# Performance work log

Hardware: AMD Instinct MI355X
Metric: run time of the kernel (lower is better)

The kernel has to match this reference:

```python
import jax, jax.numpy as jnp
import numpy as np

B, S, D = 4, 2048, 2048  # batch, seq, input_dim == state_dim
N = D

def setup_inputs() -> dict:
    key = jax.random.key(0)
    ks = jax.random.split(key, 6)
    x = jax.random.normal(ks[0], (B, S, D), dtype=jnp.float32)
    W_dt = jax.random.normal(ks[1], (N, D), dtype=jnp.float32) / np.sqrt(D)
    b_dt = jnp.ones((N,), dtype=jnp.float32)  # dt_proj.bias.fill_(1.0)
    W_B = jax.random.normal(ks[2], (N, D), dtype=jnp.float32) / np.sqrt(D)
    W_C = jax.random.normal(ks[3], (D, N), dtype=jnp.float32) / np.sqrt(N)
    A_log = jax.random.normal(ks[4], (N,), dtype=jnp.float32) * 0.5 - 1.0
    D_skip = jnp.zeros((D,), dtype=jnp.float32)
    return {"x": x, "W_dt": W_dt, "b_dt": b_dt, "W_B": W_B, "W_C": W_C,
            "A_log": A_log, "D_skip": D_skip}

def reference(x, W_dt, b_dt, W_B, W_C, A_log, D_skip):
    # dt = softplus(x @ W_dt^T + b_dt) -> [B,S,N]
    dt = jax.nn.softplus(jnp.einsum('bsd,nd->bsn', x, W_dt) + b_dt)
    Bp = jnp.einsum('bsd,nd->bsn', x, W_B)          # [B,S,N]
    A = -jnp.exp(A_log)                              # [N]
    A_bar = jnp.exp(dt * A)                          # [B,S,N]
    inputs = (dt * Bp) * x                           # B_bar * x (N == D)
    # selective scan: h_t = A_bar_t * h_{t-1} + inputs_t
    h0 = jnp.zeros((x.shape[0], A_log.shape[0]), dtype=x.dtype)
    def step(h, ab_u):
        ab, u = ab_u
        h = ab * h + u
        return h, h
    # scan over time axis: move S to leading axis
    _, h_all = jax.lax.scan(step, h0,
                            (jnp.swapaxes(A_bar, 0, 1), jnp.swapaxes(inputs, 0, 1)))
    h_all = jnp.swapaxes(h_all, 0, 1)                # [B,S,N]
    out = jnp.einsum('bsn,dn->bsd', h_all, W_C) + D_skip * x
    return out
```

## Files before the change

### kernel.cpp

```cpp
#include <hip/hip_runtime.h>

#define SEQ    2048
#define DIM    2048
#define NBATCH 4
#define MTOT   (NBATCH * SEQ)
#define CHUNKS 32
#define CLEN   (SEQ / CHUNKS)
#define NBM    (MTOT / 128)
#define TILE_E (128 * 32)

typedef __bf16 bf16_t;
typedef __bf16 bf16x8 __attribute__((ext_vector_type(8)));
typedef float  f32x4  __attribute__((ext_vector_type(4)));
typedef unsigned short u16x4 __attribute__((ext_vector_type(4)));
typedef unsigned short u16x2 __attribute__((ext_vector_type(2)));

__device__ __forceinline__ unsigned short f2bf_rne(float f) {
    unsigned int u = __float_as_uint(f);
    u += 0x7fffu + ((u >> 16) & 1u);
    return (unsigned short)(u >> 16);
}
__device__ __forceinline__ float bf2f(unsigned short v) {
    return __uint_as_float((unsigned int)v << 16);
}

__global__ void k_convert(const float* __restrict__ src,
                          unsigned short* __restrict__ dst, int n4) {
    int i = blockIdx.x * blockDim.x + threadIdx.x;
    if (i >= n4) return;
    f32x4 v = ((const f32x4*)src)[i];
    u16x4 o;
    o[0] = f2bf_rne(v[0]); o[1] = f2bf_rne(v[1]);
    o[2] = f2bf_rne(v[2]); o[3] = f2bf_rne(v[3]);
    ((u16x4*)dst)[i] = o;
}

__global__ void k_convert_ilv(const float* __restrict__ src,
                              unsigned short* __restrict__ dst, int n4, int phase) {
    int i = blockIdx.x * blockDim.x + threadIdx.x;
    if (i >= n4) return;
    const int R4 = DIM / 4;
    int nrow = i / R4;
    int dcol = i - nrow * R4;
    f32x4 v = ((const f32x4*)src)[i];
    u16x4 o;
    o[0] = f2bf_rne(v[0]); o[1] = f2bf_rne(v[1]);
    o[2] = f2bf_rne(v[2]); o[3] = f2bf_rne(v[3]);
    ((u16x4*)dst)[(2 * nrow + phase) * R4 + dcol] = o;
}

__global__ void k_prep_a(const float* __restrict__ A_log, float* __restrict__ negA, int n) {
    int i = blockIdx.x * blockDim.x + threadIdx.x;
    if (i < n) negA[i] = -__expf(A_log[i]);
}

__device__ __forceinline__ void stage_tile(const bf16_t* __restrict__ g, long rowbase,
                                           int K, int k0, bf16_t* lds,
                                           int wave, int lane) {
    const int rl     = lane >> 2;
    const int gchunk = (lane & 3) ^ ((lane >> 3) & 3);
#pragma unroll
    for (int q = 0; q < 2; q++) {
        const bf16_t* ga = g + (rowbase + wave * 32 + q * 16 + rl) * (long)K
                             + k0 + gchunk * 8;
        __builtin_amdgcn_global_load_lds(
            (const __attribute__((address_space(1))) void*)ga,
            (__attribute__((address_space(3))) void*)((char*)lds + (wave * 32 + q * 16) * 64),
            16, 0, 0);
    }
}

template <int KITERS>
__device__ __forceinline__ void gemm_main(const bf16_t* __restrict__ A,
                                          const bf16_t* __restrict__ Bm,
                                          int K, long arow0, long brow0,
                                          bf16_t* As, bf16_t* Bs,
                                          f32x4 acc[4][4],
                                          int wave, int lane, int wm, int wn) {
    const int l15  = lane & 15;
    const int quad = lane >> 4;
    const int swz  = (quad ^ ((l15 >> 1) & 3)) * 8;

    stage_tile(A,  arow0, K, 0, As, wave, lane);
    stage_tile(Bm, brow0, K, 0, Bs, wave, lane);

    for (int i = 0; i < KITERS; ++i) {
        asm volatile("s_waitcnt vmcnt(0)\n\ts_barrier" ::: "memory");
        const bf16_t* ap = As + (i & 1) * TILE_E;
        const bf16_t* bp = Bs + (i & 1) * TILE_E;
        bf16x8 af[4], bfr[4];
#pragma unroll
        for (int t = 0; t < 4; t++) {
            af[t]  = *(const bf16x8*)(ap + (wm * 64 + t * 16 + l15) * 32 + swz);
            bfr[t] = *(const bf16x8*)(bp + (wn * 64 + t * 16 + l15) * 32 + swz);
        }
        if (i + 1 < KITERS) {
            stage_tile(A,  arow0, K, (i + 1) * 32, As + ((i + 1) & 1) * TILE_E, wave, lane);
            stage_tile(Bm, brow0, K, (i + 1) * 32, Bs + ((i + 1) & 1) * TILE_E, wave, lane);
        }
#pragma unroll
        for (int t = 0; t < 4; t++)
#pragma unroll
            for (int j = 0; j < 4; j++)
                acc[t][j] = __builtin_amdgcn_mfma_f32_16x16x32_bf16(
                    af[t], bfr[j], acc[t][j], 0, 0, 0);
    }
}

__global__ __launch_bounds__(256)
void k_gemm_fused(const bf16_t* __restrict__ A, const bf16_t* __restrict__ Wcat,
                  const float* __restrict__ x, const float* __restrict__ b_dt,
                  const float* __restrict__ negA,
                  unsigned short* __restrict__ abuf, unsigned short* __restrict__ ubuf) {
    __shared__ __align__(16) bf16_t As[2 * TILE_E];
    __shared__ __align__(16) bf16_t Bs[2 * TILE_E];

    const int tid  = threadIdx.x;
    const int lane = tid & 63;
    const int wave = tid >> 6;
    const int wm   = wave >> 1;
    const int wn   = wave & 1;
    int flat = blockIdx.y * gridDim.x + blockIdx.x;
    int bm = flat % NBM;
    int bn = flat / NBM;

    f32x4 acc[4][4];
#pragma unroll
    for (int i = 0; i < 4; i++)
#pragma unroll
        for (int j = 0; j < 4; j++) acc[i][j] = (f32x4){0.f, 0.f, 0.f, 0.f};

    gemm_main<DIM / 32>(A, Wcat, DIM, (long)bm * 128, (long)bn * 128,
                        As, Bs, acc, wave, lane, wm, wn);

    const int l15  = lane & 15;
    const int quad = lane >> 4;
    const int odd  = l15 & 1;
#pragma unroll
    for (int i = 0; i < 4; i++) {
#pragma unroll
        for (int j = 0; j < 4; j++) {
#pragma unroll
            for (int r = 0; r < 4; r++) {
                float v = acc[i][j][r];
                float w = __shfl_xor(v, 1);
                float dtpre = odd ? w : v;
                float bpv   = odd ? v : w;
                long row = (long)bm * 128 + wm * 64 + i * 16 + quad * 4 + r;
                int  col = bn * 128 + wn * 64 + j * 16 + l15;
                int  n   = col >> 1;
                float z  = dtpre + b_dt[n];
                float dt = (z > 15.f) ? z : __logf(1.f + __expf(z));
                float a  = __expf(negA[n] * dt);
                float u  = dt * bpv * x[row * DIM + n];
                long idx = row * DIM + n;
                if (odd) ubuf[idx] = f2bf_rne(u); else abuf[idx] = f2bf_rne(a);
            }
        }
    }
}

__global__ __launch_bounds__(256)
void k_gemm_bt(const bf16_t* __restrict__ A, const bf16_t* __restrict__ Bm,
               float* __restrict__ C, int N, int K,
               const float* __restrict__ skip, const float* __restrict__ xres) {
    __shared__ __align__(16) bf16_t As[2 * TILE_E];
    __shared__ __align__(16) bf16_t Bs[2 * TILE_E];

    const int tid  = threadIdx.x;
    const int lane = tid & 63;
    const int wave = tid >> 6;
    const int wm   = wave >> 1;
    const int wn   = wave & 1;
    int flat = blockIdx.y * gridDim.x + blockIdx.x;
    int bm = flat % NBM;
    int bn = flat / NBM;

    f32x4 acc[4][4];
#pragma unroll
    for (int i = 0; i < 4; i++)
#pragma unroll
        for (int j = 0; j < 4; j++) acc[i][j] = (f32x4){0.f, 0.f, 0.f, 0.f};

    gemm_main<DIM / 32>(A, Bm, K, (long)bm * 128, (long)bn * 128,
                        As, Bs, acc, wave, lane, wm, wn);

    const int l15  = lane & 15;
    const int quad = lane >> 4;
#pragma unroll
    for (int i = 0; i < 4; i++) {
#pragma unroll
        for (int j = 0; j < 4; j++) {
#pragma unroll
            for (int r = 0; r < 4; r++) {
                long row = (long)bm * 128 + wm * 64 + i * 16 + quad * 4 + r;
                long col = (long)bn * 128 + wn * 64 + j * 16 + l15;
                long idx = row * (long)N + col;
                float v = acc[i][j][r];
                if (skip) v += skip[col] * xres[idx];
                C[idx] = v;
            }
        }
    }
}

__global__ void k_scan1(const unsigned short* __restrict__ a,
                        const unsigned short* __restrict__ u,
                        float* __restrict__ P, float* __restrict__ V) {
    int t  = blockIdx.x * blockDim.x + threadIdx.x;
    int n2 = t & (DIM / 2 - 1);
    int c  = (t >> 10) & (CHUNKS - 1);
    int b  = t >> 15;
    long base = ((long)b * SEQ + (long)c * CLEN) * DIM + n2 * 2;
    float p0 = 1.f, v0 = 0.f, p1 = 1.f, v1 = 0.f;
    for (int s = 0; s < CLEN; s++) {
        u16x2 av = *(const u16x2*)(a + base + (long)s * DIM);
        u16x2 uv = *(const u16x2*)(u + base + (long)s * DIM);
        float a0 = bf2f(av[0]), a1 = bf2f(av[1]);
        v0 = a0 * v0 + bf2f(uv[0]);  p0 *= a0;
        v1 = a1 * v1 + bf2f(uv[1]);  p1 *= a1;
    }
    long pidx = ((long)b * CHUNKS + c) * DIM + n2 * 2;
    *(float2*)(P + pidx) = make_float2(p0, p1);
    *(float2*)(V + pidx) = make_float2(v0, v1);
}

__global__ void k_scan2(const float* __restrict__ P, const float* __restrict__ V,
                        float* __restrict__ carry) {
    int t = blockIdx.x * blockDim.x + threadIdx.x;
    int n = t & (DIM - 1);
    int b = t >> 11;
    float H = 0.f;
    for (int c = 0; c < CHUNKS; c++) {
        long idx = ((long)b * CHUNKS + c) * DIM + n;
        carry[idx] = H;
        H = P[idx] * H + V[idx];
    }
}

__global__ void k_scan3(const unsigned short* __restrict__ a,
                        const unsigned short* __restrict__ u,
                        const float* __restrict__ carry,
                        unsigned short* __restrict__ h) {
    int t  = blockIdx.x * blockDim.x + threadIdx.x;
    int n2 = t & (DIM / 2 - 1);
    int c  = (t >> 10) & (CHUNKS - 1);
    int b  = t >> 15;
    long base = ((long)b * SEQ + (long)c * CLEN) * DIM + n2 * 2;
    long cidx = ((long)b * CHUNKS + c) * DIM + n2 * 2;
    float2 Hc = *(const float2*)(carry + cidx);
    float H0 = Hc.x, H1 = Hc.y;
    for (int s = 0; s < CLEN; s++) {
        u16x2 av = *(const u16x2*)(a + base + (long)s * DIM);
        u16x2 uv = *(const u16x2*)(u + base + (long)s * DIM);
        H0 = bf2f(av[0]) * H0 + bf2f(uv[0]);
        H1 = bf2f(av[1]) * H1 + bf2f(uv[1]);
        u16x2 o; o[0] = f2bf_rne(H0); o[1] = f2bf_rne(H1);
        *(u16x2*)(h + base + (long)s * DIM) = o;
    }
}

extern "C" void kernel_launch(void* const* d_in, const int* in_sizes, int n_in,
                              void* d_out, int out_size, void* d_ws, size_t ws_size,
                              hipStream_t stream) {
    const float* x      = (const float*)d_in[0];
    const float* W_dt   = (const float*)d_in[1];
    const float* b_dt   = (const float*)d_in[2];
    const float* W_B    = (const float*)d_in[3];
    const float* W_C    = (const float*)d_in[4];
    const float* A_log  = (const float*)d_in[5];
    const float* D_skip = (const float*)d_in[6];
    float* out = (float*)d_out;

    char* ws = (char*)d_ws;
    size_t off = 0;
    auto alloc = [&](size_t bytes) -> char* {
        char* p = ws + off;
        off += (bytes + 255) & ~(size_t)255;
        return p;
    };
    unsigned short* xb   = (unsigned short*)alloc((size_t)MTOT * DIM * 2);
    unsigned short* wcat = (unsigned short*)alloc((size_t)2 * DIM * DIM * 2);
    unsigned short* wcb  = (unsigned short*)alloc((size_t)DIM * DIM * 2);
    unsigned short* abuf = (unsigned short*)alloc((size_t)MTOT * DIM * 2);
    unsigned short* ubuf = (unsigned short*)alloc((size_t)MTOT * DIM * 2);
    float* P     = (float*)alloc((size_t)NBATCH * CHUNKS * DIM * 4);
    float* V     = (float*)alloc((size_t)NBATCH * CHUNKS * DIM * 4);
    float* carry = (float*)alloc((size_t)NBATCH * CHUNKS * DIM * 4);
    float* negA  = (float*)alloc((size_t)DIM * 4);

    const int n4x = MTOT * DIM / 4;
    const int n4w = DIM * DIM / 4;
    k_convert<<<n4x / 256, 256, 0, stream>>>(x, xb, n4x);
    k_convert_ilv<<<n4w / 256, 256, 0, stream>>>(W_dt, wcat, n4w, 0);
    k_convert_ilv<<<n4w / 256, 256, 0, stream>>>(W_B,  wcat, n4w, 1);
    k_convert<<<n4w / 256, 256, 0, stream>>>(W_C, wcb, n4w);
    k_prep_a<<<DIM / 256, 256, 0, stream>>>(A_log, negA, DIM);

    dim3 fgrid(2 * DIM / 128, MTOT / 128);
    k_gemm_fused<<<fgrid, 256, 0, stream>>>((const bf16_t*)xb, (const bf16_t*)wcat,
                                            x, b_dt, negA, abuf, ubuf);

    const int scan2_threads = NBATCH * CHUNKS * DIM / 2;
    k_scan1<<<scan2_threads / 256, 256, 0, stream>>>(abuf, ubuf, P, V);
    k_scan2<<<(NBATCH * DIM) / 256, 256, 0, stream>>>(P, V, carry);
    k_scan3<<<scan2_threads / 256, 256, 0, stream>>>(abuf, ubuf, carry, xb );

    dim3 ggrid(DIM / 128, MTOT / 128);
    k_gemm_bt<<<ggrid, 256, 0, stream>>>((const bf16_t*)xb, (const bf16_t*)wcb,
                                         out, DIM, DIM, D_skip, x);
}
```

Baseline: 558.1 us.

## Switch GEMMs to 256x256 tiles with 8-wave ping-pong pipeline and block swizzle

Both bf16 GEMMs move from 128x128 tiles with 4 waves to 256x256 tiles with 8 waves and 64-wide K steps. Global-to-LDS staging is interleaved between MFMA groups across four half-buffers with explicit vmcnt waits, barriers and setprio. Block indices are remapped so neighbouring blocks share rows of A and B for better L2 reuse. The aim is higher arithmetic intensity and overlap of loads with MFMA, at the cost of more registers and LDS per block, fewer blocks in the grid, and more intricate synchronisation.

After: 498.4 us. 1.12x faster.

```diff
diff --git a/kernel.cpp b/kernel.cpp
--- a/kernel.cpp
+++ b/kernel.cpp
@@ -6,8 +6,7 @@
 #define MTOT   (NBATCH * SEQ)
 #define CHUNKS 32
 #define CLEN   (SEQ / CHUNKS)
-#define NBM    (MTOT / 128)
-#define TILE_E (128 * 32)
+#define HT_ELEMS (256 * 32)
 
 typedef __bf16 bf16_t;
 typedef __bf16 bf16x8 __attribute__((ext_vector_type(8)));
@@ -54,7 +53,7 @@
     if (i < n) negA[i] = -__expf(A_log[i]);
 }
 
-__device__ __forceinline__ void stage_tile(const bf16_t* __restrict__ g, long rowbase,
+__device__ __forceinline__ void stage_half(const bf16_t* __restrict__ g, long rowbase,
                                            int K, int k0, bf16_t* lds,
                                            int wave, int lane) {
     const int rl     = lane >> 2;
@@ -70,74 +69,138 @@
     }
 }
 
-template <int KITERS>
-__device__ __forceinline__ void gemm_main(const bf16_t* __restrict__ A,
-                                          const bf16_t* __restrict__ Bm,
-                                          int K, long arow0, long brow0,
-                                          bf16_t* As, bf16_t* Bs,
-                                          f32x4 acc[4][4],
-                                          int wave, int lane, int wm, int wn) {
+#define MFMA_B16(a, b, c) __builtin_amdgcn_mfma_f32_16x16x32_bf16(a, b, c, 0, 0, 0)
+#define BAR_MEM asm volatile("s_barrier" ::: "memory")
+
+template <int KTILES>
+__device__ __forceinline__ void gemm256_main(const bf16_t* __restrict__ A,
+                                             const bf16_t* __restrict__ Bm,
+                                             int K, long arow0, long brow0,
+                                             bf16_t* As, bf16_t* Bs,
+                                             f32x4 acc[8][4],
+                                             int wave, int lane, int wm, int wn) {
     const int l15  = lane & 15;
     const int quad = lane >> 4;
     const int swz  = (quad ^ ((l15 >> 1) & 3)) * 8;
-
-    stage_tile(A,  arow0, K, 0, As, wave, lane);
-    stage_tile(Bm, brow0, K, 0, Bs, wave, lane);
-
-    for (int i = 0; i < KITERS; ++i) {
-        asm volatile("s_waitcnt vmcnt(0)\n\ts_barrier" ::: "memory");
-        const bf16_t* ap = As + (i & 1) * TILE_E;
-        const bf16_t* bp = Bs + (i & 1) * TILE_E;
-        bf16x8 af[4], bfr[4];
-#pragma unroll
-        for (int t = 0; t < 4; t++) {
-            af[t]  = *(const bf16x8*)(ap + (wm * 64 + t * 16 + l15) * 32 + swz);
-            bfr[t] = *(const bf16x8*)(bp + (wn * 64 + t * 16 + l15) * 32 + swz);
-        }
-        if (i + 1 < KITERS) {
-            stage_tile(A,  arow0, K, (i + 1) * 32, As + ((i + 1) & 1) * TILE_E, wave, lane);
-            stage_tile(Bm, brow0, K, (i + 1) * 32, Bs + ((i + 1) & 1) * TILE_E, wave, lane);
-        }
-#pragma unroll
-        for (int t = 0; t < 4; t++)
-#pragma unroll
-            for (int j = 0; j < 4; j++)
-                acc[t][j] = __builtin_amdgcn_mfma_f32_16x16x32_bf16(
-                    af[t], bfr[j], acc[t][j], 0, 0, 0);
-    }
-}
-
-__global__ __launch_bounds__(256)
+    const int aoff = (wm * 128 + l15) * 32 + swz;
+    const int boff = (wn * 64  + l15) * 32 + swz;
+
+    auto stA = [&](int buf, int ks, int kt) {
+        stage_half(A, arow0, K, kt * 64 + ks * 32, As + (buf * 2 + ks) * HT_ELEMS, wave, lane);
+    };
+    auto stB = [&](int buf, int ks, int kt) {
+        stage_half(Bm, brow0, K, kt * 64 + ks * 32, Bs + (buf * 2 + ks) * HT_ELEMS, wave, lane);
+    };
+
+    stB(0, 0, 0); stA(0, 0, 0); stB(0, 1, 0); stA(0, 1, 0);
+    stB(1, 0, 1); stA(1, 0, 1); stB(1, 1, 1);
+    asm volatile("s_waitcnt vmcnt(6)" ::: "memory");
+    BAR_MEM;
+
+    bf16x8 a0, a1, a2, a3, b0, b1, b2, b3;
+
+#define LDA03(BUF, KS) { const bf16_t* p = As + ((BUF) * 2 + (KS)) * HT_ELEMS + aoff; \
+    a0 = *(const bf16x8*)(p);        a1 = *(const bf16x8*)(p + 512);                  \
+    a2 = *(const bf16x8*)(p + 1024); a3 = *(const bf16x8*)(p + 1536); }
+#define LDA47(BUF, KS) { const bf16_t* p = As + ((BUF) * 2 + (KS)) * HT_ELEMS + aoff + 2048; \
+    a0 = *(const bf16x8*)(p);        a1 = *(const bf16x8*)(p + 512);                  \
+    a2 = *(const bf16x8*)(p + 1024); a3 = *(const bf16x8*)(p + 1536); }
+#define LDB(BUF, KS)  { const bf16_t* p = Bs + ((BUF) * 2 + (KS)) * HT_ELEMS + boff; \
+    b0 = *(const bf16x8*)(p);        b1 = *(const bf16x8*)(p + 512);                  \
+    b2 = *(const bf16x8*)(p + 1024); b3 = *(const bf16x8*)(p + 1536); }
+#define MM16(I0) \
+    BAR_MEM; \
+    asm volatile("s_waitcnt lgkmcnt(0)" ::: "memory"); \
+    __builtin_amdgcn_s_setprio(1); \
+    acc[(I0)+0][0] = MFMA_B16(a0, b0, acc[(I0)+0][0]); \
+    acc[(I0)+0][1] = MFMA_B16(a0, b1, acc[(I0)+0][1]); \
+    acc[(I0)+0][2] = MFMA_B16(a0, b2, acc[(I0)+0][2]); \
+    acc[(I0)+0][3] = MFMA_B16(a0, b3, acc[(I0)+0][3]); \
+    acc[(I0)+1][0] = MFMA_B16(a1, b0, acc[(I0)+1][0]); \
+    acc[(I0)+1][1] = MFMA_B16(a1, b1, acc[(I0)+1][1]); \
+    acc[(I0)+1][2] = MFMA_B16(a1, b2, acc[(I0)+1][2]); \
+    acc[(I0)+1][3] = MFMA_B16(a1, b3, acc[(I0)+1][3]); \
+    acc[(I0)+2][0] = MFMA_B16(a2, b0, acc[(I0)+2][0]); \
+    acc[(I0)+2][1] = MFMA_B16(a2, b1, acc[(I0)+2][1]); \
+    acc[(I0)+2][2] = MFMA_B16(a2, b2, acc[(I0)+2][2]); \
+    acc[(I0)+2][3] = MFMA_B16(a2, b3, acc[(I0)+2][3]); \
+    acc[(I0)+3][0] = MFMA_B16(a3, b0, acc[(I0)+3][0]); \
+    acc[(I0)+3][1] = MFMA_B16(a3, b1, acc[(I0)+3][1]); \
+    acc[(I0)+3][2] = MFMA_B16(a3, b2, acc[(I0)+3][2]); \
+    acc[(I0)+3][3] = MFMA_B16(a3, b3, acc[(I0)+3][3]); \
+    __builtin_amdgcn_s_setprio(0); \
+    BAR_MEM;
+
+#pragma unroll 1
+    for (int t = 0; t < KTILES / 2; ++t) {
+        const bool nlast = (t != KTILES / 2 - 1);
+        const int k1 = 2 * t + 1, k2 = 2 * t + 2, k3 = 2 * t + 3;
+        LDA03(0, 0); LDB(0, 0);
+        stA(1, 1, k1);
+        MM16(0);
+        LDA47(0, 0);
+        if (nlast) stB(0, 0, k2);
+        MM16(4);
+        LDA03(0, 1); LDB(0, 1);
+        if (nlast) stA(0, 0, k2);
+        MM16(0);
+        LDA47(0, 1);
+        if (nlast) stB(0, 1, k2);
+        if (nlast) { asm volatile("s_waitcnt vmcnt(6)" ::: "memory"); }
+        else       { asm volatile("s_waitcnt vmcnt(0)" ::: "memory"); }
+        MM16(4);
+        LDA03(1, 0); LDB(1, 0);
+        if (nlast) stA(0, 1, k2);
+        MM16(0);
+        LDA47(1, 0);
+        if (nlast) stB(1, 0, k3);
+        MM16(4);
+        LDA03(1, 1); LDB(1, 1);
+        if (nlast) stA(1, 0, k3);
+        MM16(0);
+        LDA47(1, 1);
+        if (nlast) stB(1, 1, k3);
+        if (nlast) { asm volatile("s_waitcnt vmcnt(6)" ::: "memory"); }
+        MM16(4);
+    }
+#undef LDA03
+#undef LDA47
+#undef LDB
+#undef MM16
+}
+
+__global__ __launch_bounds__(512, 2)
 void k_gemm_fused(const bf16_t* __restrict__ A, const bf16_t* __restrict__ Wcat,
                   const float* __restrict__ x, const float* __restrict__ b_dt,
                   const float* __restrict__ negA,
                   unsigned short* __restrict__ abuf, unsigned short* __restrict__ ubuf) {
-    __shared__ __align__(16) bf16_t As[2 * TILE_E];
-    __shared__ __align__(16) bf16_t Bs[2 * TILE_E];
+    __shared__ __align__(16) bf16_t As[4 * HT_ELEMS];
+    __shared__ __align__(16) bf16_t Bs[4 * HT_ELEMS];
 
     const int tid  = threadIdx.x;
     const int lane = tid & 63;
     const int wave = tid >> 6;
-    const int wm   = wave >> 1;
-    const int wn   = wave & 1;
-    int flat = blockIdx.y * gridDim.x + blockIdx.x;
-    int bm = flat % NBM;
-    int bn = flat / NBM;
-
-    f32x4 acc[4][4];
-#pragma unroll
-    for (int i = 0; i < 4; i++)
+    const int wm   = wave >> 2;
+    const int wn   = wave & 3;
+    int flat = blockIdx.x;
+    int swzb = (flat & 7) * 64 + (flat >> 3);
+    int bm = swzb & 31;
+    int bn = swzb >> 5;
+
+    f32x4 acc[8][4];
+#pragma unroll
+    for (int i = 0; i < 8; i++)
 #pragma unroll
         for (int j = 0; j < 4; j++) acc[i][j] = (f32x4){0.f, 0.f, 0.f, 0.f};
 
-    gemm_main<DIM / 32>(A, Wcat, DIM, (long)bm * 128, (long)bn * 128,
-                        As, Bs, acc, wave, lane, wm, wn);
+    gemm256_main<DIM / 64>(A, Wcat, DIM, (long)bm * 256, (long)bn * 256,
+                           As, Bs, acc, wave, lane, wm, wn);
 
     const int l15  = lane & 15;
     const int quad = lane >> 4;
     const int odd  = l15 & 1;
 #pragma unroll
-    for (int i = 0; i < 4; i++) {
+    for (int i = 0; i < 8; i++) {
 #pragma unroll
         for (int j = 0; j < 4; j++) {
 #pragma unroll
@@ -146,8 +209,8 @@
                 float w = __shfl_xor(v, 1);
                 float dtpre = odd ? w : v;
                 float bpv   = odd ? v : w;
-                long row = (long)bm * 128 + wm * 64 + i * 16 + quad * 4 + r;
-                int  col = bn * 128 + wn * 64 + j * 16 + l15;
+                long row = (long)bm * 256 + wm * 128 + i * 16 + quad * 4 + r;
+                int  col = bn * 256 + wn * 64 + j * 16 + l15;
                 int  n   = col >> 1;
                 float z  = dtpre + b_dt[n];
                 float dt = (z > 15.f) ? z : __logf(1.f + __expf(z));
@@ -160,41 +223,42 @@
     }
 }
 
-__global__ __launch_bounds__(256)
+__global__ __launch_bounds__(512, 2)
 void k_gemm_bt(const bf16_t* __restrict__ A, const bf16_t* __restrict__ Bm,
                float* __restrict__ C, int N, int K,
                const float* __restrict__ skip, const float* __restrict__ xres) {
-    __shared__ __align__(16) bf16_t As[2 * TILE_E];
-    __shared__ __align__(16) bf16_t Bs[2 * TILE_E];
+    __shared__ __align__(16) bf16_t As[4 * HT_ELEMS];
+    __shared__ __align__(16) bf16_t Bs[4 * HT_ELEMS];
 
     const int tid  = threadIdx.x;
     const int lane = tid & 63;
     const int wave = tid >> 6;
-    const int wm   = wave >> 1;
-    const int wn   = wave & 1;
-    int flat = blockIdx.y * gridDim.x + blockIdx.x;
-    int bm = flat % NBM;
-    int bn = flat / NBM;
-
-    f32x4 acc[4][4];
-#pragma unroll
-    for (int i = 0; i < 4; i++)
+    const int wm   = wave >> 2;
+    const int wn   = wave & 3;
+    int flat = blockIdx.x;
+    int swzb = (flat & 7) * 32 + (flat >> 3);
+    int bm = swzb & 31;
+    int bn = swzb >> 5;
+
+    f32x4 acc[8][4];
+#pragma unroll
+    for (int i = 0; i < 8; i++)
 #pragma unroll
         for (int j = 0; j < 4; j++) acc[i][j] = (f32x4){0.f, 0.f, 0.f, 0.f};
 
-    gemm_main<DIM / 32>(A, Bm, K, (long)bm * 128, (long)bn * 128,
-                        As, Bs, acc, wave, lane, wm, wn);
+    gemm256_main<DIM / 64>(A, Bm, K, (long)bm * 256, (long)bn * 256,
+                           As, Bs, acc, wave, lane, wm, wn);
 
     const int l15  = lane & 15;
     const int quad = lane >> 4;
 #pragma unroll
-    for (int i = 0; i < 4; i++) {
+    for (int i = 0; i < 8; i++) {
 #pragma unroll
         for (int j = 0; j < 4; j++) {
 #pragma unroll
             for (int r = 0; r < 4; r++) {
-                long row = (long)bm * 128 + wm * 64 + i * 16 + quad * 4 + r;
-                long col = (long)bn * 128 + wn * 64 + j * 16 + l15;
+                long row = (long)bm * 256 + wm * 128 + i * 16 + quad * 4 + r;
+                long col = (long)bn * 256 + wn * 64 + j * 16 + l15;
                 long idx = row * (long)N + col;
                 float v = acc[i][j][r];
                 if (skip) v += skip[col] * xres[idx];
@@ -297,16 +361,14 @@
     k_convert<<<n4w / 256, 256, 0, stream>>>(W_C, wcb, n4w);
     k_prep_a<<<DIM / 256, 256, 0, stream>>>(A_log, negA, DIM);
 
-    dim3 fgrid(2 * DIM / 128, MTOT / 128);
-    k_gemm_fused<<<fgrid, 256, 0, stream>>>((const bf16_t*)xb, (const bf16_t*)wcat,
-                                            x, b_dt, negA, abuf, ubuf);
+    k_gemm_fused<<<(MTOT / 256) * (2 * DIM / 256), 512, 0, stream>>>(
+        (const bf16_t*)xb, (const bf16_t*)wcat, x, b_dt, negA, abuf, ubuf);
 
     const int scan2_threads = NBATCH * CHUNKS * DIM / 2;
     k_scan1<<<scan2_threads / 256, 256, 0, stream>>>(abuf, ubuf, P, V);
     k_scan2<<<(NBATCH * DIM) / 256, 256, 0, stream>>>(P, V, carry);
     k_scan3<<<scan2_threads / 256, 256, 0, stream>>>(abuf, ubuf, carry, xb );
 
-    dim3 ggrid(DIM / 128, MTOT / 128);
-    k_gemm_bt<<<ggrid, 256, 0, stream>>>((const bf16_t*)xb, (const bf16_t*)wcb,
-                                         out, DIM, DIM, D_skip, x);
-}
+    k_gemm_bt<<<(MTOT / 256) * (DIM / 256), 512, 0, stream>>>(
+        (const bf16_t*)xb, (const bf16_t*)wcb, out, DIM, DIM, D_skip, x);
+}
```
